# Kernel tuning notes

Hardware: AMD Instinct MI355X
Metric: run time of the kernel (lower is better)

The kernel has to match this reference:

```python
import jax, jax.numpy as jnp
import numpy as np

IN_F, OUT_F, K = 512, 512, 3
UP = 1
EPS = 1e-08
LR_MUL = 1.0
PAD = (K - 1) // 2
C_EQ = LR_MUL / np.sqrt(IN_F * K * K)  # EqualizedWeight scale


def setup_inputs() -> dict:
    key = jax.random.key(0)
    k1, k2, k3, k4 = jax.random.split(key, 4)
    b, h, w = 16, 64, 64
    x = jax.random.normal(k1, (b, IN_F, h, w), dtype=jnp.float32)
    s = jax.random.uniform(k2, (b, IN_F), dtype=jnp.float32)
    weight = jax.random.normal(k3, (OUT_F, IN_F, K, K), dtype=jnp.float32)
    bias = jax.random.normal(k4, (OUT_F,), dtype=jnp.float32)
    return {"x": x, "s": s, "weight": weight, "bias": bias}


def _conv_one(xi, wi):
    # xi: [c,h,w], wi: [out,in,k,k]
    out = jax.lax.conv_general_dilated(
        xi[None], wi,
        window_strides=(1, 1),
        padding=[(PAD, PAD), (PAD, PAD)],
        dimension_numbers=("NCHW", "OIHW", "NCHW"),
    )
    return out[0]


def reference(x, s, weight, bias):
    # modulate: [b,out,in,k,k]
    w = (weight * C_EQ)[None] * s[:, None, :, None, None]
    # demodulate
    sigma_inv = jax.lax.rsqrt(jnp.sum(w * w, axis=(2, 3, 4), keepdims=True) + EPS)
    w = w * sigma_inv
    # per-sample conv (equivalent to grouped conv with groups=b)
    out = jax.vmap(_conv_one)(x, w)  # [b,out,h,w]
    out = out + (bias * LR_MUL)[None, :, None, None]
    return out
```

## Files before the change

kernel.cpp:

```cpp
#include <hip/hip_runtime.h>
#include <cstdint>

typedef unsigned short u16;
typedef __bf16 bf16x8 __attribute__((ext_vector_type(8)));
typedef float f32x4 __attribute__((ext_vector_type(4)));

#define B_    16
#define CIN   512
#define COUT  512
#define HW_   64
#define PW    66
#define XH_ELEMS  ((size_t)B_*PW*PW*CIN)
#define WBF_ELEMS ((size_t)16*9*COUT*32)

#define WAITV(N) asm volatile("s_waitcnt vmcnt(" #N ")" ::: "memory")

__device__ __forceinline__ u16 f2bf(float f) {
  union { float f; unsigned int u; } c; c.f = f;
  unsigned int u = c.u + 0x7fffu + ((c.u >> 16) & 1u);
  return (u16)(u >> 16);
}

__device__ __forceinline__ void async16(const void* g, void* l) {
  __builtin_amdgcn_global_load_lds(
      (__attribute__((address_space(1))) unsigned int*)(uintptr_t)g,
      (__attribute__((address_space(3))) unsigned int*)(uintptr_t)l,
      16, 0, 0);
}

__global__ __launch_bounds__(256) void zero_border(u16* __restrict__ xh) {
  int g = blockIdx.x * 256 + threadIdx.x;
  if (g >= B_ * 260 * 64) return;
  int c8 = g & 63;
  int t  = g >> 6;
  int b  = t / 260;
  int p  = t - b * 260;
  int rp, cp;
  if (p < 66)       { rp = 0;      cp = p; }
  else if (p < 132) { rp = 65;     cp = p - 66; }
  else {
    int q = p - 132;
    if (q < 64) { rp = q + 1;  cp = 0; }
    else        { rp = q - 63; cp = 65; }
  }
  u16* dst = xh + ((((size_t)b * PW + rp) * PW + cp) << 9) + (c8 << 3);
  *(uint4*)dst = make_uint4(0u, 0u, 0u, 0u);
}

__global__ __launch_bounds__(256) void transpose_x(const float* __restrict__ x,
                                                   const float* __restrict__ s,
                                                   u16* __restrict__ xh) {
  const int t   = threadIdx.x;
  const int c8  = t & 7;
  const int xq  = (t >> 3) & 15;
  const int y01 = t >> 7;
  const int i0  = blockIdx.x * 64;
  const int y   = blockIdx.y * 2 + y01;
  const int b   = blockIdx.z;

  const float C_EQ = 1.4731391e-2f;
  const float4 sA = *(const float4*)(s + (size_t)b * CIN + i0 + c8 * 8);
  const float4 sB = *(const float4*)(s + (size_t)b * CIN + i0 + c8 * 8 + 4);
  float cs[8] = {C_EQ * sA.x, C_EQ * sA.y, C_EQ * sA.z, C_EQ * sA.w,
                 C_EQ * sB.x, C_EQ * sB.y, C_EQ * sB.z, C_EQ * sB.w};

  float4 v[8];
#pragma unroll
  for (int k = 0; k < 8; ++k) {
    const int ci = i0 + c8 * 8 + k;
    v[k] = *(const float4*)(
        x + ((((size_t)b * CIN + ci) * HW_ + y) * HW_) + xq * 4);
  }
#pragma unroll
  for (int j = 0; j < 4; ++j) {
    const int xx = xq * 4 + j;
    u16 oc[8];
#pragma unroll
    for (int k = 0; k < 8; ++k) oc[k] = f2bf(v[k][j] * cs[k]);
    u16* dst = xh + ((((size_t)b * PW + (y + 1)) * PW + (xx + 1)) << 9)
                  + i0 + c8 * 8;
    *(uint4*)dst = *(uint4*)oc;
  }
}

__global__ __launch_bounds__(256) void sigma_kernel(const float* __restrict__ w,
                                                    const float* __restrict__ s,
                                                    float* __restrict__ sig) {
  __shared__ float row[CIN * 9];
  __shared__ float part[16][4];

  const int o   = blockIdx.x;
  const int tid = threadIdx.x;
  const int wv  = tid >> 6;
  const int lane = tid & 63;
  const float* wrow = w + (size_t)o * (CIN * 9);

#pragma unroll
  for (int it = 0; it < 5; ++it) {
    const int c = it * 256 + tid;
    if (c < 1152) *(float4*)&row[c * 4] = *(const float4*)(wrow + c * 4);
  }
  __syncthreads();

  float q0 = 0.f, q1 = 0.f;
#pragma unroll
  for (int tt = 0; tt < 9; ++tt) {
    const float a = row[(2 * tid) * 9 + tt];
    const float c = row[(2 * tid + 1) * 9 + tt];
    q0 += a * a; q1 += c * c;
  }

  const float C_EQ = 1.4731391e-2f;
#pragma unroll
  for (int b = 0; b < 16; ++b) {
    const float2 sv = *(const float2*)(s + (size_t)b * CIN + 2 * tid);
    float a = q0 * sv.x * sv.x + q1 * sv.y * sv.y;
#pragma unroll
    for (int off = 32; off > 0; off >>= 1) a += __shfl_xor(a, off, 64);
    if (lane == 0) part[b][wv] = a;
  }
  __syncthreads();
  if (tid < 16) {
    const float tot = part[tid][0] + part[tid][1] + part[tid][2] + part[tid][3];
    sig[(size_t)tid * COUT + o] = rsqrtf(tot * (C_EQ * C_EQ) + 1e-8f);
  }
}

__global__ __launch_bounds__(256) void wlayout(const float* __restrict__ w,
                                               u16* __restrict__ wbf) {
  __shared__ float wld[288][33];

  const int tid = threadIdx.x;
  const int icc = blockIdx.x & 15;
  const int oh  = blockIdx.x >> 4;
  const int o0  = oh << 5;

#pragma unroll
  for (int it = 0; it < 9; ++it) {
    const int c   = it * 256 + tid;
    const int ol  = c / 72;
    const int col = c - ol * 72;
    const float4 v = *(const float4*)(
        w + (size_t)(o0 + ol) * (CIN * 9) + icc * 288 + col * 4);
#pragma unroll
    for (int j2 = 0; j2 < 4; ++j2) wld[col * 4 + j2][ol] = v[j2];
  }
  __syncthreads();

  const int ol = tid >> 3;
  const int g4 = tid & 7;
#pragma unroll
  for (int tap = 0; tap < 9; ++tap) {
    u16 oc[4];
#pragma unroll
    for (int kk = 0; kk < 4; ++kk)
      oc[kk] = f2bf(wld[(g4 * 4 + kk) * 9 + tap][ol]);
    *(uint2*)(wbf + (((size_t)(icc * 9 + tap) * COUT) + o0 + ol) * 32 + g4 * 4)
        = *(uint2*)oc;
  }
}

#define AS_ELEMS (128 * 32)
#define BROWS    (6 * 66)
#define BS_ELEMS (BROWS * 32)

__device__ __forceinline__ void stage_A(const u16* __restrict__ wb,
                                        u16* dst, int phase, int o0, int tid) {
  const u16* asrc = wb + ((size_t)phase * COUT + o0) * 32;
#pragma unroll
  for (int t = 0; t < 2; ++t) {
    const int id   = t * 256 + tid;
    const int row  = id >> 2;
    const int slot = (id & 3) ^ (row & 3);
    async16(asrc + row * 32 + slot * 8, dst + id * 8);
  }
}

__device__ __forceinline__ void stage_B_slice(const u16* __restrict__ xb,
                                              u16* dst, int ic, int y0,
                                              int tid, int slice) {
  if (tid < 198) {
    const int id   = slice * 198 + tid;
    const int row  = id >> 2;
    const int slot = (id & 3) ^ (row & 3);
    async16(xb + ((size_t)y0 * PW + row) * CIN + ic * 32 + slot * 8,
            dst + id * 8);
  }
}

__global__ __launch_bounds__(256, 2) void modconv_mfma(const u16* __restrict__ xh,
                                                       const u16* __restrict__ wbf,
                                                       const float* __restrict__ sig,
                                                       const float* __restrict__ bias,
                                                       float* __restrict__ out) {
  __shared__ u16 As[3 * AS_ELEMS];
  __shared__ u16 Bs[2 * BS_ELEMS];

  const int tid  = threadIdx.x;
  const int lane = tid & 63;
  const int wv   = tid >> 6;
  const int l15  = lane & 15;
  const int q    = lane >> 4;
  const int sw15 = l15 & 3;

  const int lin     = blockIdx.x;
  const int logical = ((lin & 7) << 7) + (lin >> 3);
  const int yt = logical & 15;
  const int ot = (logical >> 4) & 3;
  const int b  = logical >> 6;
  const int y0 = yt << 2;
  const int o0 = ot << 7;

  const u16* xb = xh + (size_t)b * (PW * PW * CIN);
  const u16* wb = wbf;

  f32x4 acc[8][4];
#pragma unroll
  for (int mi = 0; mi < 8; ++mi)
#pragma unroll
    for (int cg = 0; cg < 4; ++cg) acc[mi][cg] = (f32x4){0.f, 0.f, 0.f, 0.f};

#pragma unroll
  for (int sl = 0; sl < 8; ++sl) stage_B_slice(xb, Bs, 0, y0, tid, sl);
  stage_A(wb, As, 0, o0, tid);
  stage_A(wb, As + AS_ELEMS, 1, o0, tid);

  for (int ic = 0; ic < 15; ++ic) {
    const int bOff = (ic & 1) * BS_ELEMS;
    const int bNxt = BS_ELEMS - bOff;
#pragma unroll
    for (int tap = 0; tap < 9; ++tap) {
      if (tap == 0) { WAITV(2); } else { WAITV(3); }
      __builtin_amdgcn_s_barrier();
      __builtin_amdgcn_sched_barrier(0);

      const int ky = tap / 3, kx = tap % 3;
      const int aCur = (tap % 3) * AS_ELEMS;
      const int aDst = ((tap + 2) % 3) * AS_ELEMS;
      const int rbbase = (wv + ky) * 66 + kx;

      bf16x8 bfr[4];
#pragma unroll
      for (int cg = 0; cg < 4; ++cg) {
        const int rb = rbbase + cg * 16 + l15;
        bfr[cg] = *(const bf16x8*)
          &Bs[bOff + (rb << 5) + ((q ^ (rb & 3)) << 3)];
      }

      stage_A(wb, As + aDst, ic * 9 + tap + 2, o0, tid);
      if (tap < 8) stage_B_slice(xb, Bs + bNxt, ic + 1, y0, tid, tap);

      __builtin_amdgcn_s_setprio(1);
#pragma unroll
      for (int mi = 0; mi < 8; ++mi) {
        const int ra = (mi << 4) + l15;
        const bf16x8 af = *(const bf16x8*)
          &As[aCur + (ra << 5) + ((q ^ sw15) << 3)];
#pragma unroll
        for (int cg = 0; cg < 4; ++cg)
          acc[mi][cg] = __builtin_amdgcn_mfma_f32_16x16x32_bf16(
              af, bfr[cg], acc[mi][cg], 0, 0, 0);
      }
      __builtin_amdgcn_s_setprio(0);
    }
  }

  {
    const int bOff = BS_ELEMS;
#pragma unroll
    for (int tap = 0; tap < 9; ++tap) {
      if (tap < 8) { WAITV(2); } else { WAITV(0); }
      __builtin_amdgcn_s_barrier();
      __builtin_amdgcn_sched_barrier(0);

      const int ky = tap / 3, kx = tap % 3;
      const int aCur = (tap % 3) * AS_ELEMS;
      const int rbbase = (wv + ky) * 66 + kx;

      bf16x8 bfr[4];
#pragma unroll
      for (int cg = 0; cg < 4; ++cg) {
        const int rb = rbbase + cg * 16 + l15;
        bfr[cg] = *(const bf16x8*)
          &Bs[bOff + (rb << 5) + ((q ^ (rb & 3)) << 3)];
      }

      if (tap <= 6)
        stage_A(wb, As + ((tap + 2) % 3) * AS_ELEMS, 135 + tap + 2, o0, tid);

      __builtin_amdgcn_s_setprio(1);
#pragma unroll
      for (int mi = 0; mi < 8; ++mi) {
        const int ra = (mi << 4) + l15;
        const bf16x8 af = *(const bf16x8*)
          &As[aCur + (ra << 5) + ((q ^ sw15) << 3)];
#pragma unroll
        for (int cg = 0; cg < 4; ++cg)
          acc[mi][cg] = __builtin_amdgcn_mfma_f32_16x16x32_bf16(
              af, bfr[cg], acc[mi][cg], 0, 0, 0);
      }
      __builtin_amdgcn_s_setprio(0);
    }
  }

  const float* sigrow = sig + (size_t)b * COUT;
  const int y = y0 + wv;
#pragma unroll
  for (int mi = 0; mi < 8; ++mi) {
#pragma unroll
    for (int rg = 0; rg < 4; ++rg) {
      const int o = o0 + (mi << 4) + (q << 2) + rg;
      const float sgv = sigrow[o];
      const float bv  = bias[o];
      const size_t base = (((size_t)b * COUT + o) * HW_ + y) * HW_;
#pragma unroll
      for (int cg = 0; cg < 4; ++cg)
        out[base + (cg << 4) + l15] = acc[mi][cg][rg] * sgv + bv;
    }
  }
}

extern "C" void kernel_launch(void* const* d_in, const int* in_sizes, int n_in,
                              void* d_out, int out_size, void* d_ws, size_t ws_size,
                              hipStream_t stream) {
  const float* x    = (const float*)d_in[0];
  const float* s    = (const float*)d_in[1];
  const float* w    = (const float*)d_in[2];
  const float* bias = (const float*)d_in[3];
  float* out = (float*)d_out;

  u16* xh    = (u16*)d_ws;
  u16* wbf   = xh + XH_ELEMS;
  float* sig = (float*)(wbf + WBF_ELEMS);

  zero_border<<<(B_ * 260 * 64 + 255) / 256, 256, 0, stream>>>(xh);
  transpose_x<<<dim3(8, 32, 16), 256, 0, stream>>>(x, s, xh);
  sigma_kernel<<<512, 256, 0, stream>>>(w, s, sig);
  wlayout<<<256, 256, 0, stream>>>(w, wbf);
  modconv_mfma<<<1024, 256, 0, stream>>>(xh, wbf, sig, bias, out);
}
```

Measured before the change: 458.8 us.

## Single-buffer B tile via register staging to raise occupancy to 3 blocks/CU

Replaces the double-buffered async global-to-LDS staging of the input tile with a register-staged prefetch: the next channel slice is loaded into registers at tap 0 and written into a single LDS buffer at the start of the next channel group. Dropping the second B buffer shrinks LDS use, and launch bounds are raised to 3 blocks per CU so more waves can hide latency. The cost is 7 extra uint4 registers per thread under a tighter register budget, an extra barrier per channel group, and prefetch that now overlaps only one channel iteration instead of being spread over taps.

New measurement: 706.3 us. +53.9%, slower.

```diff
diff --git a/kernel.cpp b/kernel.cpp
--- a/kernel.cpp
+++ b/kernel.cpp
@@ -13,7 +13,8 @@
 #define XH_ELEMS  ((size_t)B_*PW*PW*CIN)
 #define WBF_ELEMS ((size_t)16*9*COUT*32)
 
-#define WAITV(N) asm volatile("s_waitcnt vmcnt(" #N ")" ::: "memory")
+#define WAITV(N)  asm volatile("s_waitcnt vmcnt(" #N ")" ::: "memory")
+#define WAITLGKM0 asm volatile("s_waitcnt lgkmcnt(0)" ::: "memory")
 
 __device__ __forceinline__ u16 f2bf(float f) {
   union { float f; unsigned int u; } c; c.f = f;
@@ -176,25 +177,44 @@
   }
 }
 
-__device__ __forceinline__ void stage_B_slice(const u16* __restrict__ xb,
-                                              u16* dst, int ic, int y0,
-                                              int tid, int slice) {
-  if (tid < 198) {
-    const int id   = slice * 198 + tid;
+__device__ __forceinline__ void loadB(const u16* __restrict__ xb, int ic,
+                                      int y0, int tid, uint4* breg) {
+#pragma unroll
+  for (int t = 0; t < 6; ++t) {
+    const int id = t * 256 + tid;
+    breg[t] = *(const uint4*)(
+        xb + ((size_t)y0 * PW + (id >> 2)) * CIN + ic * 32 + (id & 3) * 8);
+  }
+  if (tid < 48) {
+    const int id = 1536 + tid;
+    breg[6] = *(const uint4*)(
+        xb + ((size_t)y0 * PW + (id >> 2)) * CIN + ic * 32 + (id & 3) * 8);
+  }
+}
+
+__device__ __forceinline__ void writeB(u16* Bs, int tid, const uint4* breg) {
+#pragma unroll
+  for (int t = 0; t < 6; ++t) {
+    const int id   = t * 256 + tid;
     const int row  = id >> 2;
     const int slot = (id & 3) ^ (row & 3);
-    async16(xb + ((size_t)y0 * PW + row) * CIN + ic * 32 + slot * 8,
-            dst + id * 8);
-  }
-}
-
-__global__ __launch_bounds__(256, 2) void modconv_mfma(const u16* __restrict__ xh,
+    *(uint4*)&Bs[(row << 5) + slot * 8] = breg[t];
+  }
+  if (tid < 48) {
+    const int id   = 1536 + tid;
+    const int row  = id >> 2;
+    const int slot = (id & 3) ^ (row & 3);
+    *(uint4*)&Bs[(row << 5) + slot * 8] = breg[6];
+  }
+}
+
+__global__ __launch_bounds__(256, 3) void modconv_mfma(const u16* __restrict__ xh,
                                                        const u16* __restrict__ wbf,
                                                        const float* __restrict__ sig,
                                                        const float* __restrict__ bias,
                                                        float* __restrict__ out) {
   __shared__ u16 As[3 * AS_ELEMS];
-  __shared__ u16 Bs[2 * BS_ELEMS];
+  __shared__ u16 Bs[BS_ELEMS];
 
   const int tid  = threadIdx.x;
   const int lane = tid & 63;
@@ -220,17 +240,31 @@
 #pragma unroll
     for (int cg = 0; cg < 4; ++cg) acc[mi][cg] = (f32x4){0.f, 0.f, 0.f, 0.f};
 
-#pragma unroll
-  for (int sl = 0; sl < 8; ++sl) stage_B_slice(xb, Bs, 0, y0, tid, sl);
+  uint4 breg[7];
+
+  loadB(xb, 0, y0, tid, breg);
   stage_A(wb, As, 0, o0, tid);
   stage_A(wb, As + AS_ELEMS, 1, o0, tid);
+  WAITV(4);
+  writeB(Bs, tid, breg);
+  WAITLGKM0;
 
   for (int ic = 0; ic < 15; ++ic) {
-    const int bOff = (ic & 1) * BS_ELEMS;
-    const int bNxt = BS_ELEMS - bOff;
 #pragma unroll
     for (int tap = 0; tap < 9; ++tap) {
-      if (tap == 0) { WAITV(2); } else { WAITV(3); }
+      if (tap == 0) {
+        if (ic > 0) {
+          __builtin_amdgcn_s_barrier();
+          WAITV(4);
+          writeB(Bs, tid, breg);
+          WAITLGKM0;
+        }
+        WAITV(2);
+      } else if (tap == 1 || tap == 2) {
+        WAITV(9);
+      } else {
+        WAITV(2);
+      }
       __builtin_amdgcn_s_barrier();
       __builtin_amdgcn_sched_barrier(0);
 
@@ -243,12 +277,12 @@
 #pragma unroll
       for (int cg = 0; cg < 4; ++cg) {
         const int rb = rbbase + cg * 16 + l15;
-        bfr[cg] = *(const bf16x8*)
-          &Bs[bOff + (rb << 5) + ((q ^ (rb & 3)) << 3)];
+        bfr[cg] = *(const bf16x8*)&Bs[(rb << 5) + ((q ^ (rb & 3)) << 3)];
       }
 
       stage_A(wb, As + aDst, ic * 9 + tap + 2, o0, tid);
-      if (tap < 8) stage_B_slice(xb, Bs + bNxt, ic + 1, y0, tid, tap);
+      if (tap == 0) loadB(xb, ic + 1, y0, tid, breg);
+      __builtin_amdgcn_sched_barrier(0);
 
       __builtin_amdgcn_s_setprio(1);
 #pragma unroll
@@ -266,7 +300,10 @@
   }
 
   {
-    const int bOff = BS_ELEMS;
+    __builtin_amdgcn_s_barrier();
+    WAITV(4);
+    writeB(Bs, tid, breg);
+    WAITLGKM0;
 #pragma unroll
     for (int tap = 0; tap < 9; ++tap) {
       if (tap < 8) { WAITV(2); } else { WAITV(0); }
@@ -281,8 +318,7 @@
 #pragma unroll
       for (int cg = 0; cg < 4; ++cg) {
         const int rb = rbbase + cg * 16 + l15;
-        bfr[cg] = *(const bf16x8*)
-          &Bs[bOff + (rb << 5) + ((q ^ (rb & 3)) << 3)];
+        bfr[cg] = *(const bf16x8*)&Bs[(rb << 5) + ((q ^ (rb & 3)) << 3)];
       }
 
       if (tap <= 6)
```

## Load modulated weights straight into registers and drop LDS weight buffering

Applied to the files above, without the earlier changes.

Removes the triple-buffered shared-memory staging of the weight tiles. Each wave now loads its weight fragments directly from global memory into registers, prefetching the next tap one step ahead (aC/aN). Input-tile staging is packed into the first four taps, and the per-tap barriers and vmcnt waits are replaced by one __syncthreads per input-channel chunk. The weight workspace gains one padding phase so the final prefetch stays in bounds. The intent is to cut LDS traffic and barrier stalls, at the cost of four waves redundantly fetching the same weights from cache and 32 extra VGPRs for the prefetch buffer.

After: 632.2 us. 1.38x slower.

```diff
diff --git a/kernel.cpp b/kernel.cpp
--- a/kernel.cpp
+++ b/kernel.cpp
@@ -11,9 +11,7 @@
 #define HW_   64
 #define PW    66
 #define XH_ELEMS  ((size_t)B_*PW*PW*CIN)
-#define WBF_ELEMS ((size_t)16*9*COUT*32)
-
-#define WAITV(N) asm volatile("s_waitcnt vmcnt(" #N ")" ::: "memory")
+#define WBF_ALLOC ((size_t)145*COUT*32)
 
 __device__ __forceinline__ u16 f2bf(float f) {
   union { float f; unsigned int u; } c; c.f = f;
@@ -160,21 +158,8 @@
   }
 }
 
-#define AS_ELEMS (128 * 32)
 #define BROWS    (6 * 66)
 #define BS_ELEMS (BROWS * 32)
-
-__device__ __forceinline__ void stage_A(const u16* __restrict__ wb,
-                                        u16* dst, int phase, int o0, int tid) {
-  const u16* asrc = wb + ((size_t)phase * COUT + o0) * 32;
-#pragma unroll
-  for (int t = 0; t < 2; ++t) {
-    const int id   = t * 256 + tid;
-    const int row  = id >> 2;
-    const int slot = (id & 3) ^ (row & 3);
-    async16(asrc + row * 32 + slot * 8, dst + id * 8);
-  }
-}
 
 __device__ __forceinline__ void stage_B_slice(const u16* __restrict__ xb,
                                               u16* dst, int ic, int y0,
@@ -193,7 +178,6 @@
                                                        const float* __restrict__ sig,
                                                        const float* __restrict__ bias,
                                                        float* __restrict__ out) {
-  __shared__ u16 As[3 * AS_ELEMS];
   __shared__ u16 Bs[2 * BS_ELEMS];
 
   const int tid  = threadIdx.x;
@@ -201,7 +185,6 @@
   const int wv   = tid >> 6;
   const int l15  = lane & 15;
   const int q    = lane >> 4;
-  const int sw15 = l15 & 3;
 
   const int lin     = blockIdx.x;
   const int logical = ((lin & 7) << 7) + (lin >> 3);
@@ -212,7 +195,7 @@
   const int o0 = ot << 7;
 
   const u16* xb = xh + (size_t)b * (PW * PW * CIN);
-  const u16* wb = wbf;
+  const u16* abase = wbf + ((size_t)o0 + l15) * 32 + q * 8;
 
   f32x4 acc[8][4];
 #pragma unroll
@@ -222,85 +205,52 @@
 
 #pragma unroll
   for (int sl = 0; sl < 8; ++sl) stage_B_slice(xb, Bs, 0, y0, tid, sl);
-  stage_A(wb, As, 0, o0, tid);
-  stage_A(wb, As + AS_ELEMS, 1, o0, tid);
-
-  for (int ic = 0; ic < 15; ++ic) {
+  bf16x8 aC[8];
+#pragma unroll
+  for (int mi = 0; mi < 8; ++mi)
+    aC[mi] = *(const bf16x8*)(abase + (size_t)(mi * 16) * 32);
+  __syncthreads();
+
+  for (int ic = 0; ic < 16; ++ic) {
     const int bOff = (ic & 1) * BS_ELEMS;
     const int bNxt = BS_ELEMS - bOff;
+    const int stageNext = (ic < 15);
 #pragma unroll
     for (int tap = 0; tap < 9; ++tap) {
-      if (tap == 0) { WAITV(2); } else { WAITV(3); }
-      __builtin_amdgcn_s_barrier();
-      __builtin_amdgcn_sched_barrier(0);
-
       const int ky = tap / 3, kx = tap % 3;
-      const int aCur = (tap % 3) * AS_ELEMS;
-      const int aDst = ((tap + 2) % 3) * AS_ELEMS;
       const int rbbase = (wv + ky) * 66 + kx;
 
       bf16x8 bfr[4];
 #pragma unroll
       for (int cg = 0; cg < 4; ++cg) {
         const int rb = rbbase + cg * 16 + l15;
-        bfr[cg] = *(const bf16x8*)
-          &Bs[bOff + (rb << 5) + ((q ^ (rb & 3)) << 3)];
+        bfr[cg] = *(const bf16x8*)&Bs[bOff + (rb << 5) + ((q ^ (rb & 3)) << 3)];
       }
 
-      stage_A(wb, As + aDst, ic * 9 + tap + 2, o0, tid);
-      if (tap < 8) stage_B_slice(xb, Bs + bNxt, ic + 1, y0, tid, tap);
+      const u16* ap = abase + (size_t)(ic * 9 + tap + 1) * (COUT * 32);
+      bf16x8 aN[8];
+#pragma unroll
+      for (int mi = 0; mi < 8; ++mi)
+        aN[mi] = *(const bf16x8*)(ap + (size_t)(mi * 16) * 32);
+
+      if (stageNext && tap < 4) {
+        stage_B_slice(xb, Bs + bNxt, ic + 1, y0, tid, 2 * tap);
+        stage_B_slice(xb, Bs + bNxt, ic + 1, y0, tid, 2 * tap + 1);
+      }
 
       __builtin_amdgcn_s_setprio(1);
 #pragma unroll
-      for (int mi = 0; mi < 8; ++mi) {
-        const int ra = (mi << 4) + l15;
-        const bf16x8 af = *(const bf16x8*)
-          &As[aCur + (ra << 5) + ((q ^ sw15) << 3)];
+      for (int mi = 0; mi < 8; ++mi)
 #pragma unroll
         for (int cg = 0; cg < 4; ++cg)
           acc[mi][cg] = __builtin_amdgcn_mfma_f32_16x16x32_bf16(
-              af, bfr[cg], acc[mi][cg], 0, 0, 0);
-      }
+              aC[mi], bfr[cg], acc[mi][cg], 0, 0, 0);
       __builtin_amdgcn_s_setprio(0);
+
+#pragma unroll
+      for (int mi = 0; mi < 8; ++mi) aC[mi] = aN[mi];
     }
-  }
-
-  {
-    const int bOff = BS_ELEMS;
-#pragma unroll
-    for (int tap = 0; tap < 9; ++tap) {
-      if (tap < 8) { WAITV(2); } else { WAITV(0); }
-      __builtin_amdgcn_s_barrier();
-      __builtin_amdgcn_sched_barrier(0);
-
-      const int ky = tap / 3, kx = tap % 3;
-      const int aCur = (tap % 3) * AS_ELEMS;
-      const int rbbase = (wv + ky) * 66 + kx;
-
-      bf16x8 bfr[4];
-#pragma unroll
-      for (int cg = 0; cg < 4; ++cg) {
-        const int rb = rbbase + cg * 16 + l15;
-        bfr[cg] = *(const bf16x8*)
-          &Bs[bOff + (rb << 5) + ((q ^ (rb & 3)) << 3)];
-      }
-
-      if (tap <= 6)
-        stage_A(wb, As + ((tap + 2) % 3) * AS_ELEMS, 135 + tap + 2, o0, tid);
-
-      __builtin_amdgcn_s_setprio(1);
-#pragma unroll
-      for (int mi = 0; mi < 8; ++mi) {
-        const int ra = (mi << 4) + l15;
-        const bf16x8 af = *(const bf16x8*)
-          &As[aCur + (ra << 5) + ((q ^ sw15) << 3)];
-#pragma unroll
-        for (int cg = 0; cg < 4; ++cg)
-          acc[mi][cg] = __builtin_amdgcn_mfma_f32_16x16x32_bf16(
-              af, bfr[cg], acc[mi][cg], 0, 0, 0);
-      }
-      __builtin_amdgcn_s_setprio(0);
-    }
+    __syncthreads();
   }
 
   const float* sigrow = sig + (size_t)b * COUT;
@@ -331,7 +281,7 @@
 
   u16* xh    = (u16*)d_ws;
   u16* wbf   = xh + XH_ELEMS;
-  float* sig = (float*)(wbf + WBF_ELEMS);
+  float* sig = (float*)(wbf + WBF_ALLOC);
 
   zero_border<<<(B_ * 260 * 64 + 255) / 256, 256, 0, stream>>>(xh);
   transpose_x<<<dim3(8, 32, 16), 256, 0, stream>>>(x, s, xh);
```
